# Kernel optimization log

Measured on AMD Instinct MI355X. Metric: run time of the kernel, lower is better.

## Reference

```python
import jax, jax.numpy as jnp
import numpy as np

B, S, H, D = 32, 127, 4, 64
HD = H * D
SCALE = 1.0 / np.sqrt(D).astype(np.float32)
NEG = -100000.0


def _remove_mask_keep(seq_len):
    # For q>=3, rows are grouped in 2-row blocks starting at i=3,5,...;
    # each block may only attend (among k>=3) to its own two columns.
    q = jnp.arange(seq_len)[:, None]
    k = jnp.arange(seq_len)[None, :]
    blk = 3 + 2 * ((q - 3) // 2)
    return (q < 3) | (k < 3) | ((k >= blk) & (k < blk + 2))  # [S, S] bool


def setup_inputs() -> dict:
    rng = jax.random.key(0)
    ks = jax.random.split(rng, 16)
    n = lambda k, shape: jax.random.normal(k, shape, dtype=jnp.float32)
    w = 1.0 / np.sqrt(HD).astype(np.float32)
    return {
        "query": n(ks[0], (B, S, HD)),
        "key": n(ks[1], (B, S, HD)),
        "value": n(ks[2], (B, S, HD)),
        "graph": jax.random.randint(ks[3], (B, S, S), 0, 2, dtype=jnp.int32),
        "edge_key": n(ks[4], (B, S, S, D)),
        "edge_value": n(ks[5], (B, S, S, D)),
        "edge_query": n(ks[6], (B, S, S, D)),
        "Wq": n(ks[7], (HD, HD)) * w, "bq": jnp.zeros((HD,), jnp.float32),
        "Wk": n(ks[8], (HD, HD)) * w, "bk": jnp.zeros((HD,), jnp.float32),
        "Wv": n(ks[9], (HD, HD)) * w, "bv": jnp.zeros((HD,), jnp.float32),
        "Wo": n(ks[10], (HD, HD)) * w, "bo": jnp.zeros((HD,), jnp.float32),
    }


def reference(query, key, value, graph, edge_key, edge_value, edge_query,
              Wq, bq, Wk, bk, Wv, bv, Wo, bo):
    b, s, _ = query.shape
    q = (query @ Wq.T + bq).reshape(b, s, H, D)
    k = (key @ Wk.T + bk).reshape(b, s, H, D)
    v = (value @ Wv.T + bv).reshape(b, s, H, D)

    scores = (
        jnp.einsum('bqhd,bkhd->bhqk', q, k)
        + jnp.einsum('bqhd,bqkd->bhqk', q, edge_key)
        + jnp.einsum('bkqd,bkhd->bhqk', edge_query, k)
        + jnp.einsum('bkqd,bqkd->bqk', edge_query, edge_key)[:, None]
    ) * SCALE

    mask = (graph != 0)[:, None, :, :] & _remove_mask_keep(s)[None, None]
    scores = jnp.where(mask, scores, NEG)
    attn = jax.nn.softmax(scores, axis=-1)  # dropout p=0 -> identity

    x = (jnp.einsum('bhqk,bkhd->bqhd', attn, v)
         + jnp.einsum('bhqk,bqkd->bqhd', attn, edge_value)).reshape(b, s, HD)
    return x @ Wo.T + bo
```

## Files before the change

### kernel.cpp

```cpp
#include <hip/hip_runtime.h>
#include <hip/hip_bf16.h>

#define S_LEN 127
#define NB    32
#define HDIM  256
#define DH    64
#define SCALE_F 0.125f

typedef __bf16 bf16x8 __attribute__((ext_vector_type(8)));
typedef __bf16 bf16x4 __attribute__((ext_vector_type(4)));
typedef float  f32x4  __attribute__((ext_vector_type(4)));

#define NTOK  4064
#define NQKV4 260096
#define NW4   16384

__global__ __launch_bounds__(256) void convert_bf16(
    const float* __restrict__ q, const float* __restrict__ k,
    const float* __restrict__ v,
    const float* __restrict__ Wq, const float* __restrict__ Wk,
    const float* __restrict__ Wv, const float* __restrict__ Wo,
    __bf16* __restrict__ qb, __bf16* __restrict__ kb, __bf16* __restrict__ vb,
    __bf16* __restrict__ Wqb, __bf16* __restrict__ Wkb,
    __bf16* __restrict__ Wvb, __bf16* __restrict__ Wob)
{
  size_t t = (size_t)blockIdx.x * 256 + threadIdx.x;
  const float* src; __bf16* dst;
  if (t < NQKV4)               { src = q;  dst = qb;  }
  else if ((t -= NQKV4) < NQKV4) { src = k;  dst = kb;  }
  else if ((t -= NQKV4) < NQKV4) { src = v;  dst = vb;  }
  else if ((t -= NQKV4) < NW4)   { src = Wq; dst = Wqb; }
  else if ((t -= NW4) < NW4)     { src = Wk; dst = Wkb; }
  else if ((t -= NW4) < NW4)     { src = Wv; dst = Wvb; }
  else if ((t -= NW4) < NW4)     { src = Wo; dst = Wob; }
  else return;
  const float4 x = ((const float4*)src)[t];
  bf16x4 r;
  r[0] = (__bf16)x.x; r[1] = (__bf16)x.y; r[2] = (__bf16)x.z; r[3] = (__bf16)x.w;
  ((bf16x4*)dst)[t] = r;
}

__device__ __forceinline__ void gemm_tile32_bf16(
    const __bf16* __restrict__ A, const __bf16* __restrict__ W,
    const float* __restrict__ bias, float* __restrict__ out,
    int row0, int col0)
{
  const int lane = threadIdx.x & 63;
  const int r  = lane & 15;
  const int ks = (lane >> 4) << 3;
  const __bf16* Ab = A + (size_t)(row0 + r) * HDIM + ks;
  const __bf16* Wb = W + (size_t)(col0 + r) * HDIM + ks;
  f32x4 acc[2][2] = {};

  bf16x8 ca[2], cw[2];
  ca[0] = *(const bf16x8*)Ab;
  ca[1] = *(const bf16x8*)(Ab + (size_t)16 * HDIM);
  cw[0] = *(const bf16x8*)Wb;
  cw[1] = *(const bf16x8*)(Wb + (size_t)16 * HDIM);
#pragma unroll
  for (int kb = 0; kb < 8; ++kb) {
    bf16x8 na[2], nw[2];
    if (kb < 7) {
      const int off = (kb + 1) * 32;
      na[0] = *(const bf16x8*)(Ab + off);
      na[1] = *(const bf16x8*)(Ab + (size_t)16 * HDIM + off);
      nw[0] = *(const bf16x8*)(Wb + off);
      nw[1] = *(const bf16x8*)(Wb + (size_t)16 * HDIM + off);
    }
#pragma unroll
    for (int mi = 0; mi < 2; ++mi)
#pragma unroll
      for (int ni = 0; ni < 2; ++ni)
        acc[mi][ni] = __builtin_amdgcn_mfma_f32_16x16x32_bf16(
            ca[mi], cw[ni], acc[mi][ni], 0, 0, 0);
    if (kb < 7) {
      ca[0] = na[0]; ca[1] = na[1];
      cw[0] = nw[0]; cw[1] = nw[1];
    }
  }
  const int crow = (lane >> 4) * 4;
  const int ccol = lane & 15;
#pragma unroll
  for (int mi = 0; mi < 2; ++mi)
#pragma unroll
    for (int ni = 0; ni < 2; ++ni) {
      const int oc = col0 + ni * 16 + ccol;
      const float bv = bias[oc];
#pragma unroll
      for (int rg = 0; rg < 4; ++rg)
        out[(size_t)(row0 + mi * 16 + crow + rg) * HDIM + oc] = acc[mi][ni][rg] + bv;
    }
}

__global__ __launch_bounds__(256) void gemm_qkv(
    const __bf16* __restrict__ qb, const __bf16* __restrict__ kb,
    const __bf16* __restrict__ vb,
    const __bf16* __restrict__ Wqb, const float* __restrict__ bq,
    const __bf16* __restrict__ Wkb, const float* __restrict__ bk,
    const __bf16* __restrict__ Wvb, const float* __restrict__ bv,
    float* __restrict__ qp, float* __restrict__ kp, float* __restrict__ vp)
{
  const int w = threadIdx.x >> 6;
  const int tile = blockIdx.x * 4 + w;
  if (tile >= 127) return;
  const __bf16* A; const __bf16* W; const float* bias; float* o;
  if (blockIdx.z == 0)      { A = qb; W = Wqb; bias = bq; o = qp; }
  else if (blockIdx.z == 1) { A = kb; W = Wkb; bias = bk; o = kp; }
  else                      { A = vb; W = Wvb; bias = bv; o = vp; }
  gemm_tile32_bf16(A, W, bias, o, tile * 32, blockIdx.y * 32);
}

__global__ __launch_bounds__(256) void gemm_o(
    const __bf16* __restrict__ A, const __bf16* __restrict__ W,
    const float* __restrict__ bias, float* __restrict__ out)
{
  const int w = threadIdx.x >> 6;
  const int tile = blockIdx.x * 4 + w;
  if (tile >= 127) return;
  gemm_tile32_bf16(A, W, bias, out, tile * 32, blockIdx.y * 32);
}

__global__ __launch_bounds__(256) void attn_kernel(
    const float* __restrict__ qp, const float* __restrict__ kp,
    const float* __restrict__ vp, const int* __restrict__ graph,
    const float* __restrict__ ekt, const float* __restrict__ evt,
    const float* __restrict__ eqt, __bf16* __restrict__ xpb)
{
  int b, q;
  {
    const int bx = blockIdx.x;
    if (bx < 96) { b = bx / 3; q = bx % 3; }
    else { const int rr = bx - 96; b = rr / 124; q = 3 + rr % 124; }
  }
  const int t = threadIdx.x;
  const int w = t >> 6;
  const int l = t & 63;

  __shared__ int   s_list[S_LEN];
  __shared__ float s_attn[4][S_LEN];
  __shared__ int   s_cnt[2];

  bool valid = false;
  const int k0 = w * 64 + l;
  if (w < 2 && k0 < S_LEN) {
    const int g = graph[((size_t)b * S_LEN + q) * S_LEN + k0];
    bool keep;
    if (q < 3 || k0 < 3) keep = true;
    else {
      const int blk = 3 + 2 * ((q - 3) >> 1);
      keep = (k0 >= blk) & (k0 < blk + 2);
    }
    valid = (g != 0) && keep;
  }
  const unsigned long long bal = __ballot(valid);
  if (w < 2 && l == 0) s_cnt[w] = (int)__popcll(bal);
  __syncthreads();
  int n = s_cnt[0] + s_cnt[1];
  if (valid) {
    const int pos = (int)__popcll(bal & ((1ull << l) - 1ull)) + (w ? s_cnt[0] : 0);
    s_list[pos] = k0;
  }
  __syncthreads();

  if (n == 0) {
    if (t < S_LEN) {
      s_list[t] = t;
      const float u = 1.0f / 127.0f;
      s_attn[0][t] = u; s_attn[1][t] = u; s_attn[2][t] = u; s_attn[3][t] = u;
    }
    n = S_LEN;
  } else {
    const float* qrow = qp + ((size_t)b * S_LEN + q) * HDIM;
    const float  q0 = qrow[l], q1 = qrow[64 + l], q2 = qrow[128 + l], q3 = qrow[192 + l];
    const float* eqb = eqt + ((size_t)b * S_LEN * S_LEN + q) * DH;
    const float* ekb = ekt + ((size_t)(b * S_LEN + q)) * S_LEN * DH;
    const float* kpb = kp + (size_t)b * S_LEN * HDIM;

    float ceq = 0.f, cek = 0.f, ck0 = 0.f, ck1 = 0.f, ck2 = 0.f, ck3 = 0.f;
    if (w < n) {
      const int kk = s_list[w];
      ceq = eqb[(size_t)kk * (S_LEN * DH) + l];
      cek = ekb[kk * DH + l];
      const float* kr = kpb + (size_t)kk * HDIM;
      ck0 = kr[l]; ck1 = kr[64 + l]; ck2 = kr[128 + l]; ck3 = kr[192 + l];
    }
    for (int i0 = 0; i0 < n; i0 += 4) {
      const int i = i0 + w;
      float neq = 0.f, nek = 0.f, nk0 = 0.f, nk1 = 0.f, nk2 = 0.f, nk3 = 0.f;
      const int j = i + 4;
      if (j < n) {
        const int kk = s_list[j];
        neq = eqb[(size_t)kk * (S_LEN * DH) + l];
        nek = ekb[kk * DH + l];
        const float* kr = kpb + (size_t)kk * HDIM;
        nk0 = kr[l]; nk1 = kr[64 + l]; nk2 = kr[128 + l]; nk3 = kr[192 + l];
      }
      float p0 = (q0 + ceq) * (ck0 + cek);
      float p1 = (q1 + ceq) * (ck1 + cek);
      float p2 = (q2 + ceq) * (ck2 + cek);
      float p3 = (q3 + ceq) * (ck3 + cek);
#pragma unroll
      for (int off = 32; off; off >>= 1) {
        p0 += __shfl_xor(p0, off, 64);
        p1 += __shfl_xor(p1, off, 64);
        p2 += __shfl_xor(p2, off, 64);
        p3 += __shfl_xor(p3, off, 64);
      }
      if (i < n && l < 4) {
        const float s = (l == 0) ? p0 : (l == 1) ? p1 : (l == 2) ? p2 : p3;
        s_attn[l][i] = s * SCALE_F;
      }
      ceq = neq; cek = nek; ck0 = nk0; ck1 = nk1; ck2 = nk2; ck3 = nk3;
    }
    __syncthreads();

    {
      const float v0 = (l < n) ? s_attn[w][l] : -INFINITY;
      const float v1 = (64 + l < n) ? s_attn[w][64 + l] : -INFINITY;
      float mx = fmaxf(v0, v1);
#pragma unroll
      for (int off = 32; off; off >>= 1) mx = fmaxf(mx, __shfl_xor(mx, off, 64));
      const float e0 = (l < n) ? expf(v0 - mx) : 0.f;
      const float e1 = (64 + l < n) ? expf(v1 - mx) : 0.f;
      float sm = e0 + e1;
#pragma unroll
      for (int off = 32; off; off >>= 1) sm += __shfl_xor(sm, off, 64);
      const float inv = 1.0f / sm;
      if (l < n) s_attn[w][l] = e0 * inv;
      if (64 + l < n) s_attn[w][64 + l] = e1 * inv;
    }
  }
  __syncthreads();

  {
    const float* evb = evt + ((size_t)(b * S_LEN + q)) * S_LEN * DH;
    const float* vbp = vp + (size_t)b * S_LEN * HDIM + w * DH;
    float acc0 = 0.f, acc1 = 0.f;
    int i = 0;
    for (; i + 4 <= n; i += 4) {
      const int ka = s_list[i], kb2 = s_list[i + 1];
      const int kc = s_list[i + 2], kd = s_list[i + 3];
      const float aa = s_attn[w][i],     ab = s_attn[w][i + 1];
      const float ac = s_attn[w][i + 2], ad = s_attn[w][i + 3];
      const float va = vbp[(size_t)ka * HDIM + l],   ea = evb[ka * DH + l];
      const float vb2 = vbp[(size_t)kb2 * HDIM + l], eb = evb[kb2 * DH + l];
      const float vc = vbp[(size_t)kc * HDIM + l],   ec = evb[kc * DH + l];
      const float vd = vbp[(size_t)kd * HDIM + l],   ed = evb[kd * DH + l];
      acc0 += aa * (va + ea) + ab * (vb2 + eb);
      acc1 += ac * (vc + ec) + ad * (vd + ed);
    }
    for (; i < n; ++i) {
      const int kk = s_list[i];
      acc0 += s_attn[w][i] * (vbp[(size_t)kk * HDIM + l] + evb[kk * DH + l]);
    }
    xpb[((size_t)b * S_LEN + q) * HDIM + t] = (__bf16)(acc0 + acc1);
  }
}

extern "C" void kernel_launch(void* const* d_in, const int* in_sizes, int n_in,
                              void* d_out, int out_size, void* d_ws, size_t ws_size,
                              hipStream_t stream) {
  const float* query = (const float*)d_in[0];
  const float* key   = (const float*)d_in[1];
  const float* value = (const float*)d_in[2];
  const int*   graph = (const int*)d_in[3];
  const float* ekt   = (const float*)d_in[4];
  const float* evt   = (const float*)d_in[5];
  const float* eqt   = (const float*)d_in[6];
  const float* Wq = (const float*)d_in[7];  const float* bq = (const float*)d_in[8];
  const float* Wk = (const float*)d_in[9];  const float* bk = (const float*)d_in[10];
  const float* Wv = (const float*)d_in[11]; const float* bv = (const float*)d_in[12];
  const float* Wo = (const float*)d_in[13]; const float* bo = (const float*)d_in[14];
  float* out = (float*)d_out;

  const size_t NE = (size_t)NTOK * HDIM;
  char* p = (char*)d_ws;
  float* qp = (float*)p;            p += NE * 4;
  float* kp = (float*)p;            p += NE * 4;
  float* vp = (float*)p;            p += NE * 4;
  __bf16* qb  = (__bf16*)p;         p += NE * 2;
  __bf16* kb  = (__bf16*)p;         p += NE * 2;
  __bf16* vb  = (__bf16*)p;         p += NE * 2;
  __bf16* xpb = (__bf16*)p;         p += NE * 2;
  __bf16* Wqb = (__bf16*)p;         p += (size_t)HDIM * HDIM * 2;
  __bf16* Wkb = (__bf16*)p;         p += (size_t)HDIM * HDIM * 2;
  __bf16* Wvb = (__bf16*)p;         p += (size_t)HDIM * HDIM * 2;
  __bf16* Wob = (__bf16*)p;

  convert_bf16<<<dim3(3304), 256, 0, stream>>>(query, key, value,
                                               Wq, Wk, Wv, Wo,
                                               qb, kb, vb, Wqb, Wkb, Wvb, Wob);
  gemm_qkv<<<dim3(32, 8, 3), 256, 0, stream>>>(qb, kb, vb,
                                               Wqb, bq, Wkb, bk, Wvb, bv,
                                               qp, kp, vp);
  attn_kernel<<<dim3(NB * S_LEN), 256, 0, stream>>>(qp, kp, vp, graph,
                                                    ekt, evt, eqt, xpb);
  gemm_o<<<dim3(32, 8), 256, 0, stream>>>(xpb, Wob, bo, out);
}
```

Before: 54.34 us.

## Vectorize attention kernel with float4 loads and 16-lane key groups

Restructures the score phase so each wave processes four keys at once, with 16 lanes per key each loading float4 chunks of edge_query, edge_key and the projected key rows. The reduction now covers 16 lanes instead of 64. The weighted-sum phase also uses float4 loads over four keys per wave, then a cross-group shuffle reduction and a packed bf16x4 store. This cuts load instruction count and shuffle depth but drops the explicit software prefetch of the next key.

```diff
diff --git a/kernel.cpp b/kernel.cpp
--- a/kernel.cpp
+++ b/kernel.cpp
@@ -135,6 +135,8 @@
   const int t = threadIdx.x;
   const int w = t >> 6;
   const int l = t & 63;
+  const int ll = l & 15;
+  const int g  = l >> 4;
 
   __shared__ int   s_list[S_LEN];
   __shared__ float s_attn[4][S_LEN];
@@ -143,14 +145,14 @@
   bool valid = false;
   const int k0 = w * 64 + l;
   if (w < 2 && k0 < S_LEN) {
-    const int g = graph[((size_t)b * S_LEN + q) * S_LEN + k0];
+    const int gr = graph[((size_t)b * S_LEN + q) * S_LEN + k0];
     bool keep;
     if (q < 3 || k0 < 3) keep = true;
     else {
       const int blk = 3 + 2 * ((q - 3) >> 1);
       keep = (k0 >= blk) & (k0 < blk + 2);
     }
-    valid = (g != 0) && keep;
+    valid = (gr != 0) && keep;
   }
   const unsigned long long bal = __ballot(valid);
   if (w < 2 && l == 0) s_cnt[w] = (int)__popcll(bal);
@@ -171,46 +173,51 @@
     n = S_LEN;
   } else {
     const float* qrow = qp + ((size_t)b * S_LEN + q) * HDIM;
-    const float  q0 = qrow[l], q1 = qrow[64 + l], q2 = qrow[128 + l], q3 = qrow[192 + l];
+    float4 q4[4];
+#pragma unroll
+    for (int h = 0; h < 4; ++h)
+      q4[h] = *(const float4*)(qrow + h * 64 + ll * 4);
     const float* eqb = eqt + ((size_t)b * S_LEN * S_LEN + q) * DH;
     const float* ekb = ekt + ((size_t)(b * S_LEN + q)) * S_LEN * DH;
     const float* kpb = kp + (size_t)b * S_LEN * HDIM;
 
-    float ceq = 0.f, cek = 0.f, ck0 = 0.f, ck1 = 0.f, ck2 = 0.f, ck3 = 0.f;
-    if (w < n) {
-      const int kk = s_list[w];
-      ceq = eqb[(size_t)kk * (S_LEN * DH) + l];
-      cek = ekb[kk * DH + l];
-      const float* kr = kpb + (size_t)kk * HDIM;
-      ck0 = kr[l]; ck1 = kr[64 + l]; ck2 = kr[128 + l]; ck3 = kr[192 + l];
-    }
-    for (int i0 = 0; i0 < n; i0 += 4) {
-      const int i = i0 + w;
-      float neq = 0.f, nek = 0.f, nk0 = 0.f, nk1 = 0.f, nk2 = 0.f, nk3 = 0.f;
-      const int j = i + 4;
-      if (j < n) {
-        const int kk = s_list[j];
-        neq = eqb[(size_t)kk * (S_LEN * DH) + l];
-        nek = ekb[kk * DH + l];
-        const float* kr = kpb + (size_t)kk * HDIM;
-        nk0 = kr[l]; nk1 = kr[64 + l]; nk2 = kr[128 + l]; nk3 = kr[192 + l];
+    for (int i0 = 0; i0 < n; i0 += 16) {
+      const int i = i0 + w * 4 + g;
+      float p0 = 0.f, p1 = 0.f, p2 = 0.f, p3 = 0.f;
+      if (i < n) {
+        const int kk = s_list[i];
+        const float4 eq4 = *(const float4*)(eqb + (size_t)kk * (S_LEN * DH) + ll * 4);
+        const float4 ek4 = *(const float4*)(ekb + kk * DH + ll * 4);
+        const float* kr = kpb + (size_t)kk * HDIM + ll * 4;
+        const float4 kh0 = *(const float4*)(kr);
+        const float4 kh1 = *(const float4*)(kr + 64);
+        const float4 kh2 = *(const float4*)(kr + 128);
+        const float4 kh3 = *(const float4*)(kr + 192);
+        const float tx = ek4.x, ty = ek4.y, tz = ek4.z, tw = ek4.w;
+        const float s0x = q4[0].x + eq4.x, s0y = q4[0].y + eq4.y,
+                    s0z = q4[0].z + eq4.z, s0w = q4[0].w + eq4.w;
+        const float s1x = q4[1].x + eq4.x, s1y = q4[1].y + eq4.y,
+                    s1z = q4[1].z + eq4.z, s1w = q4[1].w + eq4.w;
+        const float s2x = q4[2].x + eq4.x, s2y = q4[2].y + eq4.y,
+                    s2z = q4[2].z + eq4.z, s2w = q4[2].w + eq4.w;
+        const float s3x = q4[3].x + eq4.x, s3y = q4[3].y + eq4.y,
+                    s3z = q4[3].z + eq4.z, s3w = q4[3].w + eq4.w;
+        p0 = s0x*(kh0.x+tx) + s0y*(kh0.y+ty) + s0z*(kh0.z+tz) + s0w*(kh0.w+tw);
+        p1 = s1x*(kh1.x+tx) + s1y*(kh1.y+ty) + s1z*(kh1.z+tz) + s1w*(kh1.w+tw);
+        p2 = s2x*(kh2.x+tx) + s2y*(kh2.y+ty) + s2z*(kh2.z+tz) + s2w*(kh2.w+tw);
+        p3 = s3x*(kh3.x+tx) + s3y*(kh3.y+ty) + s3z*(kh3.z+tz) + s3w*(kh3.w+tw);
       }
-      float p0 = (q0 + ceq) * (ck0 + cek);
-      float p1 = (q1 + ceq) * (ck1 + cek);
-      float p2 = (q2 + ceq) * (ck2 + cek);
-      float p3 = (q3 + ceq) * (ck3 + cek);
-#pragma unroll
-      for (int off = 32; off; off >>= 1) {
+#pragma unroll
+      for (int off = 1; off < 16; off <<= 1) {
         p0 += __shfl_xor(p0, off, 64);
         p1 += __shfl_xor(p1, off, 64);
         p2 += __shfl_xor(p2, off, 64);
         p3 += __shfl_xor(p3, off, 64);
       }
-      if (i < n && l < 4) {
-        const float s = (l == 0) ? p0 : (l == 1) ? p1 : (l == 2) ? p2 : p3;
-        s_attn[l][i] = s * SCALE_F;
+      if (i < n && ll < 4) {
+        const float s = (ll == 0) ? p0 : (ll == 1) ? p1 : (ll == 2) ? p2 : p3;
+        s_attn[ll][i] = s * SCALE_F;
       }
-      ceq = neq; cek = nek; ck0 = nk0; ck1 = nk1; ck2 = nk2; ck3 = nk3;
     }
     __syncthreads();
 
@@ -234,26 +241,33 @@
 
   {
     const float* evb = evt + ((size_t)(b * S_LEN + q)) * S_LEN * DH;
-    const float* vbp = vp + (size_t)b * S_LEN * HDIM + w * DH;
-    float acc0 = 0.f, acc1 = 0.f;
-    int i = 0;
-    for (; i + 4 <= n; i += 4) {
-      const int ka = s_list[i], kb2 = s_list[i + 1];
-      const int kc = s_list[i + 2], kd = s_list[i + 3];
-      const float aa = s_attn[w][i],     ab = s_attn[w][i + 1];
-      const float ac = s_attn[w][i + 2], ad = s_attn[w][i + 3];
-      const float va = vbp[(size_t)ka * HDIM + l],   ea = evb[ka * DH + l];
-      const float vb2 = vbp[(size_t)kb2 * HDIM + l], eb = evb[kb2 * DH + l];
-      const float vc = vbp[(size_t)kc * HDIM + l],   ec = evb[kc * DH + l];
-      const float vd = vbp[(size_t)kd * HDIM + l],   ed = evb[kd * DH + l];
-      acc0 += aa * (va + ea) + ab * (vb2 + eb);
-      acc1 += ac * (vc + ec) + ad * (vd + ed);
-    }
-    for (; i < n; ++i) {
-      const int kk = s_list[i];
-      acc0 += s_attn[w][i] * (vbp[(size_t)kk * HDIM + l] + evb[kk * DH + l]);
-    }
-    xpb[((size_t)b * S_LEN + q) * HDIM + t] = (__bf16)(acc0 + acc1);
+    const float* vbp = vp + (size_t)b * S_LEN * HDIM + w * DH + ll * 4;
+    float ax = 0.f, ay = 0.f, az = 0.f, aw = 0.f;
+    for (int i0 = 0; i0 < n; i0 += 4) {
+      const int i = i0 + g;
+      if (i < n) {
+        const int kk = s_list[i];
+        const float a = s_attn[w][i];
+        const float4 v4 = *(const float4*)(vbp + (size_t)kk * HDIM);
+        const float4 e4 = *(const float4*)(evb + kk * DH + ll * 4);
+        ax += a * (v4.x + e4.x);
+        ay += a * (v4.y + e4.y);
+        az += a * (v4.z + e4.z);
+        aw += a * (v4.w + e4.w);
+      }
+    }
+#pragma unroll
+    for (int off = 16; off < 64; off <<= 1) {
+      ax += __shfl_xor(ax, off, 64);
+      ay += __shfl_xor(ay, off, 64);
+      az += __shfl_xor(az, off, 64);
+      aw += __shfl_xor(aw, off, 64);
+    }
+    if (g == 0) {
+      bf16x4 r;
+      r[0] = (__bf16)ax; r[1] = (__bf16)ay; r[2] = (__bf16)az; r[3] = (__bf16)aw;
+      *(bf16x4*)(xpb + ((size_t)b * S_LEN + q) * HDIM + w * 64 + ll * 4) = r;
+    }
   }
 }
 
```

Measured after the change: 52.76 us. -2.9%, faster.
